# Performance work log

Measured on AMD Instinct MI355X. Metric: run time of the kernel, lower is better.

The kernel has to match this reference:

```python
import jax, jax.numpy as jnp
import numpy as np

VOCAB, N_ENT, N_FACT, D = 32000, 64, 512, 512
B, L = 128, 128


def setup_inputs() -> dict:
    key = jax.random.key(0)
    k1, k2, k3, k4, k5 = jax.random.split(key, 5)
    caption_indices = jax.random.randint(k1, (B, L), 0, VOCAB + N_ENT + N_FACT, dtype=jnp.int64 if jax.config.read('jax_enable_x64') else jnp.int32)
    entities_encoded = jax.random.normal(k2, (B, N_ENT, D), dtype=jnp.float32)
    facts_encoded = jax.random.normal(k3, (B, N_FACT, D), dtype=jnp.float32)
    word_embedding = jax.random.normal(k4, (VOCAB, D), dtype=jnp.float32)
    caption_masks = jax.random.randint(k5, (B, L, 1), 0, 3)
    return {
        'caption_indices': caption_indices,
        'entities_encoded': entities_encoded,
        'facts_encoded': facts_encoded,
        'word_embedding': word_embedding,
        'pad_token': 0,
        'caption_masks': caption_masks,
    }


def reference(caption_indices, entities_encoded, facts_encoded, word_embedding, pad_token, caption_masks):
    vocab = word_embedding.shape[0]
    n_ent = entities_encoded.shape[1]
    n_fact = facts_encoded.shape[1]

    # entity indices: offset by vocab, clamp invalid to last entity slot
    ent_idx = caption_indices - vocab
    ent_idx = jnp.where((ent_idx < 0) | (ent_idx >= n_ent), n_ent - 1, ent_idx)
    # fact indices: offset by vocab + n_ent, clamp invalid to last fact slot
    fact_idx = caption_indices - vocab - n_ent
    fact_idx = jnp.where((fact_idx < 0) | (fact_idx >= n_fact), n_fact - 1, fact_idx)
    # word indices: anything >= vocab becomes pad
    word_idx = jnp.where(caption_indices >= vocab, pad_token, caption_indices)

    emb_words = word_embedding[word_idx]                                    # [B, L, D]
    emb_ents = jnp.take_along_axis(entities_encoded, ent_idx[:, :, None], axis=1)   # [B, L, D]
    emb_facts = jnp.take_along_axis(facts_encoded, fact_idx[:, :, None], axis=1)    # [B, L, D]

    tmp = jnp.where(caption_masks == 1, emb_ents, emb_words)
    return jnp.where(caption_masks == 2, emb_facts, tmp)
```

## Files before the change

### kernel.cpp

```cpp
#include <hip/hip_runtime.h>


constexpr int VOCAB  = 32000;
constexpr int N_ENT  = 64;
constexpr int N_FACT = 512;
constexpr int D      = 512;
constexpr int L      = 128;

constexpr int VEC = 4;
constexpr int TPR = D / VEC;
constexpr int BLOCK = 256;

__global__ __launch_bounds__(BLOCK) void caption_embed_kernel(
    const int*    __restrict__ idx,
    const float4* __restrict__ ents,
    const float4* __restrict__ facts,
    const float4* __restrict__ words,
    const int*    __restrict__ pad_tok,
    const int*    __restrict__ masks,
    float4*       __restrict__ out,
    int n_rows)
{
    const int tid = blockIdx.x * BLOCK + threadIdx.x;
    const int row = tid / TPR;
    const int col = tid % TPR;
    if (row >= n_rows) return;

    const int b  = row / L;
    const int ci = idx[row];
    const int m  = masks[row];

    const float4* src;
    long src_row;
    if (m == 1) {
        int e = ci - VOCAB;
        if (e < 0 || e >= N_ENT) e = N_ENT - 1;
        src = ents;
        src_row = (long)b * N_ENT + e;
    } else if (m == 2) {
        int f = ci - VOCAB - N_ENT;
        if (f < 0 || f >= N_FACT) f = N_FACT - 1;
        src = facts;
        src_row = (long)b * N_FACT + f;
    } else {
        int w = (ci >= VOCAB) ? pad_tok[0] : ci;
        src = words;
        src_row = w;
    }

    out[(long)row * TPR + col] = src[src_row * TPR + col];
}

extern "C" void kernel_launch(void* const* d_in, const int* in_sizes, int n_in,
                              void* d_out, int out_size, void* d_ws, size_t ws_size,
                              hipStream_t stream) {
    const int*    idx     = (const int*)d_in[0];
    const float4* ents    = (const float4*)d_in[1];
    const float4* facts   = (const float4*)d_in[2];
    const float4* words   = (const float4*)d_in[3];
    const int*    pad_tok = (const int*)d_in[4];
    const int*    masks   = (const int*)d_in[5];
    float4*       out     = (float4*)d_out;

    const int n_rows = in_sizes[0];
    const int total  = n_rows * TPR;
    const int grid   = (total + BLOCK - 1) / BLOCK;

    caption_embed_kernel<<<grid, BLOCK, 0, stream>>>(
        idx, ents, facts, words, pad_tok, masks, out, n_rows);
}
```

Baseline: 13.90 us.

## Map one wavefront per row with scalar row index and nontemporal stores

Assigns one 64-lane wavefront per output row, and each lane copies two 16-byte vectors, so the grid shrinks by half. The row index is made wave-uniform with readfirstlane, which lets the index, mask and source selection run on the scalar unit instead of per lane. Output writes use nontemporal stores so the streamed result does not pollute the cache. The bounds check is removed and the grid assumes n_rows*64 is divisible by the block size, which holds for these shapes.

```diff
diff --git a/kernel.cpp b/kernel.cpp
--- a/kernel.cpp
+++ b/kernel.cpp
@@ -7,65 +7,69 @@
 constexpr int D      = 512;
 constexpr int L      = 128;
 
-constexpr int VEC = 4;
-constexpr int TPR = D / VEC;
+typedef float f32x4 __attribute__((ext_vector_type(4)));
+
+constexpr int TPR   = 64;
 constexpr int BLOCK = 256;
 
 __global__ __launch_bounds__(BLOCK) void caption_embed_kernel(
-    const int*    __restrict__ idx,
-    const float4* __restrict__ ents,
-    const float4* __restrict__ facts,
-    const float4* __restrict__ words,
-    const int*    __restrict__ pad_tok,
-    const int*    __restrict__ masks,
-    float4*       __restrict__ out,
-    int n_rows)
+    const int*   __restrict__ idx,
+    const f32x4* __restrict__ ents,
+    const f32x4* __restrict__ facts,
+    const f32x4* __restrict__ words,
+    const int*   __restrict__ pad_tok,
+    const int*   __restrict__ masks,
+    f32x4*       __restrict__ out)
 {
     const int tid = blockIdx.x * BLOCK + threadIdx.x;
-    const int row = tid / TPR;
-    const int col = tid % TPR;
-    if (row >= n_rows) return;
+    const int row = __builtin_amdgcn_readfirstlane(tid >> 6);
+    const int col = threadIdx.x & 63;
 
-    const int b  = row / L;
+    const int b  = row >> 7;
     const int ci = idx[row];
     const int m  = masks[row];
 
-    const float4* src;
-    long src_row;
+    const f32x4* src;
+    int src_row;
     if (m == 1) {
         int e = ci - VOCAB;
         if (e < 0 || e >= N_ENT) e = N_ENT - 1;
-        src = ents;
-        src_row = (long)b * N_ENT + e;
+        src = ents + (long)b * (N_ENT * (D / 4));
+        src_row = e;
     } else if (m == 2) {
         int f = ci - VOCAB - N_ENT;
         if (f < 0 || f >= N_FACT) f = N_FACT - 1;
-        src = facts;
-        src_row = (long)b * N_FACT + f;
+        src = facts + (long)b * (N_FACT * (D / 4));
+        src_row = f;
     } else {
         int w = (ci >= VOCAB) ? pad_tok[0] : ci;
         src = words;
         src_row = w;
     }
 
-    out[(long)row * TPR + col] = src[src_row * TPR + col];
+    const f32x4* s = src + (long)src_row * (D / 4) + col;
+    f32x4*       d = out + (long)row * (D / 4) + col;
+
+    f32x4 v0 = s[0];
+    f32x4 v1 = s[64];
+    __builtin_nontemporal_store(v0, d);
+    __builtin_nontemporal_store(v1, d + 64);
 }
 
 extern "C" void kernel_launch(void* const* d_in, const int* in_sizes, int n_in,
                               void* d_out, int out_size, void* d_ws, size_t ws_size,
                               hipStream_t stream) {
-    const int*    idx     = (const int*)d_in[0];
-    const float4* ents    = (const float4*)d_in[1];
-    const float4* facts   = (const float4*)d_in[2];
-    const float4* words   = (const float4*)d_in[3];
-    const int*    pad_tok = (const int*)d_in[4];
-    const int*    masks   = (const int*)d_in[5];
-    float4*       out     = (float4*)d_out;
+    const int*   idx     = (const int*)d_in[0];
+    const f32x4* ents    = (const f32x4*)d_in[1];
+    const f32x4* facts   = (const f32x4*)d_in[2];
+    const f32x4* words   = (const f32x4*)d_in[3];
+    const int*   pad_tok = (const int*)d_in[4];
+    const int*   masks   = (const int*)d_in[5];
+    f32x4*       out     = (f32x4*)d_out;
 
     const int n_rows = in_sizes[0];
-    const int total  = n_rows * TPR;
-    const int grid   = (total + BLOCK - 1) / BLOCK;
+    const int grid   = n_rows * TPR / BLOCK;
 
     caption_embed_kernel<<<grid, BLOCK, 0, stream>>>(
-        idx, ents, facts, words, pad_tok, masks, out, n_rows);
+        idx, ents, facts, words, pad_tok, masks, out);
 }
```

New measurement: 16.36 us. 1.18x slower.
